# Performance work log

Hardware: AMD Instinct MI355X
Metric: run time of the kernel (lower is better)

## Reference

```python
import jax, jax.numpy as jnp
import numpy as np

# Module hyperparameters (from init_kwargs)
CUTOFF = 10.0
K = 32            # max_num_neighbors
N = 8192          # number of atoms
B = 32            # number of molecules
BOX = 32.0        # box side length -> realistic neighbor density for cutoff=10


def setup_inputs() -> dict:
    key = jax.random.key(0)
    k1, k2 = jax.random.split(key)
    pos = jax.random.uniform(k1, (N, 3), dtype=jnp.float32) * BOX
    batch = jnp.sort(jax.random.randint(k2, (N,), 0, B, dtype=jnp.int32))
    return {"pos": pos, "batch": batch}


def reference(pos, batch):
    """radius_graph(pos, r=CUTOFF, batch, loop=False, max_num_neighbors=K)
    followed by edge_weight = ||pos[row] - pos[col]||.
    Fixed-size output: up to K edges per target node; padding edges are
    self-loops (src == tgt) with edge_weight == 0.
    """
    n = pos.shape[0]
    # Pairwise squared distances via Gram trick: [N, N], no [N,N,3] intermediate.
    sq = jnp.sum(pos * pos, axis=-1)
    d2 = sq[:, None] + sq[None, :] - 2.0 * (pos @ pos.T)
    same_mol = batch[:, None] == batch[None, :]
    not_self = ~jnp.eye(n, dtype=bool)  # loop=False
    mask = same_mol & not_self & (d2 <= CUTOFF * CUTOFF)

    # Cap at K neighbors per target node: take the K nearest valid candidates.
    neg = jnp.where(mask, -d2, -jnp.inf)
    vals, src = jax.lax.top_k(neg, K)          # [N, K]
    valid = vals > -jnp.inf                    # [N, K]
    tgt = jnp.broadcast_to(jnp.arange(n, dtype=src.dtype)[:, None], (n, K))
    src = jnp.where(valid, src, tgt)           # pad with self-index

    row = src.reshape(-1)                      # source nodes  [N*K]
    col = tgt.reshape(-1)                      # target nodes  [N*K]
    vflat = valid.reshape(-1)

    diff = pos[row] - pos[col]                 # gather + pairwise delta
    d2e = jnp.sum(diff * diff, axis=-1)
    # safe sqrt (padding rows have d2e == 0; avoid NaN grads by masking input)
    edge_weight = jnp.where(vflat, jnp.sqrt(jnp.where(vflat, d2e, 1.0)), 0.0)

    edge_index = jnp.stack([row, col])         # [2, N*K], flow=source_to_target
    return edge_index, edge_weight
```

## Files before the change

### kernel.cpp

```cpp
#include <hip/hip_runtime.h>
#include <math.h>


#define KNBR 32
#define CUT2 100.0f
#define MAXT 8

typedef unsigned long long u64;

__device__ __forceinline__ u64 shfl_xor_u64(u64 v, int m) {
  int lo = __shfl_xor((int)(unsigned)(v & 0xffffffffull), m, 64);
  int hi = __shfl_xor((int)(unsigned)(v >> 32), m, 64);
  return ((u64)(unsigned)hi << 32) | (unsigned)lo;
}
__device__ __forceinline__ u64 shfl_u64(u64 v, int src) {
  int lo = __shfl((int)(unsigned)(v & 0xffffffffull), src, 64);
  int hi = __shfl((int)(unsigned)(v >> 32), src, 64);
  return ((u64)(unsigned)hi << 32) | (unsigned)lo;
}
__device__ __forceinline__ u64 permute_u64(int dest, u64 v) {
  const int addr = dest << 2;
  int lo = __builtin_amdgcn_ds_permute(addr, (int)(unsigned)(v & 0xffffffffull));
  int hi = __builtin_amdgcn_ds_permute(addr, (int)(unsigned)(v >> 32));
  return ((u64)(unsigned)hi << 32) | (unsigned)lo;
}
__device__ __forceinline__ u64 bitonic_sort64(u64 key, const int lane) {
#pragma unroll
  for (int k = 2; k <= 64; k <<= 1) {
#pragma unroll
    for (int j = k >> 1; j > 0; j >>= 1) {
      const u64 o = shfl_xor_u64(key, j);
      const bool lower = (lane & j) == 0;
      const bool up = (lane & k) == 0;
      const u64 mn = key < o ? key : o;
      const u64 mx = key < o ? o : key;
      key = (lower == up) ? mn : mx;
    }
  }
  return key;
}
__device__ __forceinline__ unsigned order_bits(float f) {
  const unsigned b = __float_as_uint(f);
  return b ^ ((b & 0x80000000u) ? 0xffffffffu : 0x80000000u);
}

__global__ __launch_bounds__(256) void radius_graph_kernel(
    const float* __restrict__ pos, const int* __restrict__ batch,
    float* __restrict__ out, const int n) {
  const int wave = threadIdx.x >> 6;
  const int lane = threadIdx.x & 63;
  const int i = (blockIdx.x << 2) + wave;
  if (i >= n) return;

  const float xi = pos[3 * i + 0], yi = pos[3 * i + 1], zi = pos[3 * i + 2];
  const float sq_i =
      __fadd_rn(__fadd_rn(__fmul_rn(xi, xi), __fmul_rn(yi, yi)), __fmul_rn(zi, zi));
  const int m = batch[i];

  {
  }
  const int skey = m + (lane & 1);
  int lo = 0, hi = n;
  while (lo < hi) {
    const int mid = (lo + hi) >> 1;
    if (batch[mid] < skey) lo = mid + 1; else hi = mid;
  }
  const int s = __shfl(lo, 0);
  const int e = __shfl(lo, 1);
  const int cnt = e - s;

  float d2r[MAXT];
  u64 r0 = ~0ull;
  int count = 0;
  u64 vxor = 0, vsum = 0;
#pragma unroll
  for (int t = 0; t < MAXT; ++t) {
    const int c = (t << 6) + lane;
    float d2 = INFINITY;
    bool valid = false;
    u64 key = ~0ull;
    if (c < cnt) {
      const int j = s + c;
      const float xj = pos[3 * j + 0], yj = pos[3 * j + 1], zj = pos[3 * j + 2];
      const float sq_j =
          __fadd_rn(__fadd_rn(__fmul_rn(xj, xj), __fmul_rn(yj, yj)), __fmul_rn(zj, zj));
      float dot = __fmul_rn(xi, xj);
      dot = __builtin_fmaf(yi, yj, dot);
      dot = __builtin_fmaf(zi, zj, dot);
      const float dd = __fsub_rn(__fadd_rn(sq_i, sq_j), __fmul_rn(2.0f, dot));
      if (j != i && dd <= CUT2) {
        d2 = dd;
        valid = true;
        key = ((u64)order_bits(dd) << 32) | (unsigned)c;
        vxor ^= key;
        vsum += key;
      }
    }
    d2r[t] = d2;
    const u64 bmask = __ballot(valid);
    const int sv = (int)__popcll(bmask);
    const int below = (int)__popcll(bmask & ((1ull << lane) - 1ull));
    const int dest =
        (valid ? (count + below) : (count + sv + (lane - below))) & 63;
    const u64 perm = permute_u64(dest, key);
    const bool take = (lane >= count) && (lane < count + sv);
    r0 = take ? perm : r0;
    count += sv;
  }

  int sel_src = i;
  int sel_valid = 0;
  bool good = false;
  if (count <= 64) {
    const u64 a = bitonic_sort64(r0, lane);
    const u64 prev = shfl_u64(a, lane - 1);
    const bool lane_ok = (lane == 0) || (prev <= a);
    u64 dx = vxor ^ ((a != ~0ull) ? a : 0);
    u64 ds = vsum - ((a != ~0ull) ? a : 0);
#pragma unroll
    for (int off = 32; off; off >>= 1) {
      dx ^= shfl_xor_u64(dx, off);
      ds += shfl_xor_u64(ds, off);
    }
    good = __all(lane_ok && (dx == 0) && (ds == 0));
    if (good && lane < KNBR && a != ~0ull) {
      sel_valid = 1;
      sel_src = s + (int)(unsigned)(a & 0xffffffffull);
    }
  }

  if (!good) {
    unsigned used = 0;
    for (int k = 0; k < KNBR; ++k) {
      float best = INFINITY;
      int bestc = 0x7fffffff;
#pragma unroll
      for (int t = 0; t < MAXT; ++t) {
        const int c = (t << 6) + lane;
        const float v = d2r[t];
        if (!((used >> t) & 1u) &&
            (v < best || (v == best && v < INFINITY && c < bestc))) {
          best = v;
          bestc = c;
        }
      }
#pragma unroll
      for (int off = 32; off; off >>= 1) {
        const float ov = __shfl_xor(best, off);
        const int oc = __shfl_xor(bestc, off);
        if (ov < best || (ov == best && oc < bestc)) { best = ov; bestc = oc; }
      }
      const bool sel = best < INFINITY;
      if (!sel) break;
      if ((bestc & 63) == lane) used |= 1u << (bestc >> 6);
      if (lane == k) { sel_src = s + bestc; sel_valid = 1; }
    }
  }

  if (lane < KNBR) {
    float w = 0.0f;
    if (sel_valid) {
      const float xj = pos[3 * sel_src + 0], yj = pos[3 * sel_src + 1],
                  zj = pos[3 * sel_src + 2];
      const float dx2 = __fsub_rn(xj, xi), dy2 = __fsub_rn(yj, yi),
                  dz2 = __fsub_rn(zj, zi);
      const float d2e = __fadd_rn(
          __fadd_rn(__fmul_rn(dx2, dx2), __fmul_rn(dy2, dy2)), __fmul_rn(dz2, dz2));
      w = sqrtf(d2e);
    }
    const size_t nk = (size_t)n * KNBR;
    const size_t base = (size_t)i * KNBR + lane;
    out[base] = (float)sel_src;
    out[nk + base] = (float)i;
    out[2 * nk + base] = w;
  }
}

extern "C" void kernel_launch(void* const* d_in, const int* in_sizes, int n_in,
                              void* d_out, int out_size, void* d_ws, size_t ws_size,
                              hipStream_t stream) {
  const float* pos = (const float*)d_in[0];
  const int* batch = (const int*)d_in[1];
  float* out = (float*)d_out;
  const int n = in_sizes[0] / 3;
  const int blocks = (n + 3) / 4;
  radius_graph_kernel<<<blocks, 256, 0, stream>>>(pos, batch, out, n);
}
```

Baseline: 18.25 us.

## Use wave-parallel 3-level segment search and reuse Gram distance for edge weight

Replaces the per-lane serial binary search for molecule segment bounds with a three-level, wave-wide parallel search (stride 256, 8, 1) that uses ballots, with a validated fallback to the old binary search. Edge weights now take the square root of the Gram-trick squared distance already stored in the sort key, so the final pos gather and recomputation are dropped. This cuts the dependent global-load latency chains. The risk is that weights computed from the Gram form can differ numerically from the reference's direct difference formula.

Result: faster. 17.68 us (-3.1%).

```diff
diff --git a/kernel.cpp b/kernel.cpp
--- a/kernel.cpp
+++ b/kernel.cpp
@@ -57,16 +57,53 @@
       __fadd_rn(__fadd_rn(__fmul_rn(xi, xi), __fmul_rn(yi, yi)), __fmul_rn(zi, zi));
   const int m = batch[i];
 
+  const int kkey = m + (lane >> 5);
+  const int hl = lane & 31;
+  int lo_s = 0, lo_e = 0;
   {
-  }
-  const int skey = m + (lane & 1);
-  int lo = 0, hi = n;
-  while (lo < hi) {
-    const int mid = (lo + hi) >> 1;
-    if (batch[mid] < skey) lo = mid + 1; else hi = mid;
-  }
-  const int s = __shfl(lo, 0);
-  const int e = __shfl(lo, 1);
+    const int myLo = (lane < 32) ? lo_s : lo_e;
+    const int p = myLo + (hl << 8);
+    const bool lt = (p < n) && (batch[p < n ? p : n - 1] < kkey);
+    const u64 bm = __ballot(lt);
+    const int cs = (int)__popcll(bm & 0xffffffffull);
+    const int ce = (int)__popcll(bm >> 32);
+    lo_s += (cs == 0) ? 0 : ((cs - 1) << 8) + 1;
+    lo_e += (ce == 0) ? 0 : ((ce - 1) << 8) + 1;
+  }
+  {
+    const int myLo = (lane < 32) ? lo_s : lo_e;
+    const int p = myLo + (hl << 3);
+    const bool lt = (p < n) && (batch[p < n ? p : n - 1] < kkey);
+    const u64 bm = __ballot(lt);
+    const int cs = (int)__popcll(bm & 0xffffffffull);
+    const int ce = (int)__popcll(bm >> 32);
+    lo_s += (cs == 0) ? 0 : ((cs - 1) << 3) + 1;
+    lo_e += (ce == 0) ? 0 : ((ce - 1) << 3) + 1;
+  }
+  int s, e;
+  {
+    const int myLo = (lane < 32) ? lo_s : lo_e;
+    const int p = myLo + hl;
+    const bool lt = (p < n) && (batch[p < n ? p : n - 1] < kkey);
+    const u64 bm = __ballot(lt);
+    s = lo_s + (int)__popcll(bm & 0xffffffffull);
+    e = lo_e + (int)__popcll(bm >> 32);
+  }
+  bool se_ok = (s >= 0) && (s < e) && (e <= n);
+  if (se_ok) {
+    se_ok = (batch[s] == m) && (s == 0 || batch[s - 1] < m) &&
+            (batch[e - 1] == m) && (e == n || batch[e] > m);
+  }
+  if (!se_ok) {
+    const int skey2 = m + (lane & 1);
+    int blo = 0, bhi = n;
+    while (blo < bhi) {
+      const int mid = (blo + bhi) >> 1;
+      if (batch[mid] < skey2) blo = mid + 1; else bhi = mid;
+    }
+    s = __shfl(blo, 0);
+    e = __shfl(blo, 1);
+  }
   const int cnt = e - s;
 
   float d2r[MAXT];
@@ -110,6 +147,7 @@
 
   int sel_src = i;
   int sel_valid = 0;
+  float sel_d2 = 0.0f;
   bool good = false;
   if (count <= 64) {
     const u64 a = bitonic_sort64(r0, lane);
@@ -126,6 +164,8 @@
     if (good && lane < KNBR && a != ~0ull) {
       sel_valid = 1;
       sel_src = s + (int)(unsigned)(a & 0xffffffffull);
+      const unsigned xb = (unsigned)(a >> 32);
+      sel_d2 = __uint_as_float((xb & 0x80000000u) ? (xb ^ 0x80000000u) : ~xb);
     }
   }
 
@@ -153,21 +193,12 @@
       const bool sel = best < INFINITY;
       if (!sel) break;
       if ((bestc & 63) == lane) used |= 1u << (bestc >> 6);
-      if (lane == k) { sel_src = s + bestc; sel_valid = 1; }
+      if (lane == k) { sel_src = s + bestc; sel_valid = 1; sel_d2 = best; }
     }
   }
 
   if (lane < KNBR) {
-    float w = 0.0f;
-    if (sel_valid) {
-      const float xj = pos[3 * sel_src + 0], yj = pos[3 * sel_src + 1],
-                  zj = pos[3 * sel_src + 2];
-      const float dx2 = __fsub_rn(xj, xi), dy2 = __fsub_rn(yj, yi),
-                  dz2 = __fsub_rn(zj, zi);
-      const float d2e = __fadd_rn(
-          __fadd_rn(__fmul_rn(dx2, dx2), __fmul_rn(dy2, dy2)), __fmul_rn(dz2, dz2));
-      w = sqrtf(d2e);
-    }
+    const float w = sel_valid ? sqrtf(sel_d2) : 0.0f;
     const size_t nk = (size_t)n * KNBR;
     const size_t base = (size_t)i * KNBR + lane;
     out[base] = (float)sel_src;
```
